# Kernel tuning notes

Hardware: AMD Instinct MI355X
Metric: run time of the kernel (lower is better)

The kernel has to match this reference:

```python
import jax, jax.numpy as jnp
import numpy as np
import math

HIDDEN = 1024
HEADS = 16
HEAD_DIM = HIDDEN // HEADS


def setup_inputs() -> dict:
    key = jax.random.key(0)
    ks = jax.random.split(key, 9)
    B, T, C = 4, 2048, HIDDEN
    s = 0.02
    x = jax.random.normal(ks[0], (B, T, C), dtype=jnp.float32)
    # torch nn.Linear weights are [out_features, in_features]
    Wq = jax.random.normal(ks[1], (C, C), dtype=jnp.float32) * s
    Wk = jax.random.normal(ks[2], (C, C), dtype=jnp.float32) * s
    Wv = jax.random.normal(ks[3], (C, C), dtype=jnp.float32) * s
    Wo = jax.random.normal(ks[4], (C, C), dtype=jnp.float32) * s
    bq = jax.random.normal(ks[5], (C,), dtype=jnp.float32) * s
    bk = jax.random.normal(ks[6], (C,), dtype=jnp.float32) * s
    bv = jax.random.normal(ks[7], (C,), dtype=jnp.float32) * s
    bo = jax.random.normal(ks[8], (C,), dtype=jnp.float32) * s
    return {"x": x, "Wq": Wq, "bq": bq, "Wk": Wk, "bk": bk,
            "Wv": Wv, "bv": bv, "Wo": Wo, "bo": bo}


def reference(x, Wq, bq, Wk, bk, Wv, bv, Wo, bo):
    B, T, C = x.shape
    H, D = HEADS, HEAD_DIM
    # projections: torch Linear => x @ W.T + b
    q = (x @ Wq.T + bq).reshape(B, T, H, D).transpose(0, 2, 1, 3)  # [B,H,T,D]
    k = (x @ Wk.T + bk).reshape(B, T, H, D).transpose(0, 2, 1, 3)
    v = (x @ Wv.T + bv).reshape(B, T, H, D).transpose(0, 2, 1, 3)
    scale = 1.0 / math.sqrt(D)
    scores = jnp.einsum('bhqd,bhkd->bhqk', q, k) * scale  # [B,H,T,T]
    attn = jax.nn.softmax(scores, axis=-1)
    y = jnp.einsum('bhqk,bhkd->bhqd', attn, v)  # [B,H,T,D]
    y = y.transpose(0, 2, 1, 3).reshape(B, T, C)
    return y @ Wo.T + bo
```

## Files before the change

### kernel.cpp

```cpp
#include <hip/hip_runtime.h>
#include <stdint.h>


using u16 = unsigned short;
using u32 = unsigned int;
typedef __attribute__((ext_vector_type(8)))  __bf16 bf16x8;
typedef __attribute__((ext_vector_type(4)))  float  floatx4;
typedef __attribute__((ext_vector_type(16))) float  f32x16;
typedef __attribute__((ext_vector_type(2)))  unsigned int u32x2;

#define QSCALE 0.18033688011112043f

__device__ __forceinline__ u16 f2b(float f) {
    union { float f; u32 i; } x; x.f = f;
    return (u16)((x.i + 0x7fffu + ((x.i >> 16) & 1u)) >> 16);
}
__device__ __forceinline__ u32 fbits(float f) { union { float f; u32 i; } x; x.f = f; return x.i; }
__device__ __forceinline__ u32 pkbf(float a, float b) {
    u32 ia = fbits(a) + 0x8000u, ib = fbits(b) + 0x8000u;
    return __builtin_amdgcn_perm(ib, ia, 0x07060302u);
}
__device__ __forceinline__ u32 cvtpk(float a, float b) {
    u32 r; asm("v_cvt_pk_bf16_f32 %0, %1, %2" : "=v"(r) : "v"(a), "v"(b)); return r;
}
__device__ __forceinline__ bf16x8 ld16B(const u16* p) {
    bf16x8 v; __builtin_memcpy(&v, p, 16); return v;
}
__device__ __forceinline__ void async16(const u16* g, u16* l) {
    __builtin_amdgcn_global_load_lds((const __attribute__((address_space(1))) unsigned int*)g,
                                     (__attribute__((address_space(3))) unsigned int*)l,
                                     16, 0, 0);
}

__global__ __launch_bounds__(256) void convert_kernel(
    const float* __restrict__ x,
    const float* __restrict__ Wq, const float* __restrict__ Wk,
    const float* __restrict__ Wv, const float* __restrict__ Wo,
    u16* __restrict__ xb, u16* __restrict__ wqb, u16* __restrict__ wkb,
    u16* __restrict__ wvb, u16* __restrict__ wob)
{
    size_t e = ((size_t)blockIdx.x * 256 + threadIdx.x) * 4;
    const float* src; u16* dst; size_t off;
    const size_t XN = (size_t)8 << 20;
    if (e < XN) { src = x; dst = xb; off = e; }
    else {
        size_t k = e - XN;
        int w = (int)(k >> 20);
        off = k & ((1u << 20) - 1);
        src = (w == 0) ? Wq : (w == 1) ? Wk : (w == 2) ? Wv : Wo;
        dst = (w == 0) ? wqb : (w == 1) ? wkb : (w == 2) ? wvb : wob;
    }
    float4 f = *(const float4*)(src + off);
    u32 dws[2] = { pkbf(f.x, f.y), pkbf(f.z, f.w) };
    __builtin_memcpy(dst + off, dws, 8);
}

__device__ __forceinline__ void gemm_loop(const u16* __restrict__ A, const u16* __restrict__ W,
                                          int m0, int n0, floatx4 (&acc)[4][4],
                                          u16* __restrict__ sA, u16* __restrict__ sB)
{
    constexpr int K = 1024;
    const int tid  = threadIdx.x;
    const int wave = tid >> 6, lane = tid & 63;
    const int wr = wave >> 1, wc = wave & 1;
    const int quad = lane >> 4, l15 = lane & 15;

    #pragma unroll
    for (int i = 0; i < 4; ++i)
        #pragma unroll
        for (int j = 0; j < 4; ++j)
            acc[i][j] = (floatx4){0.f, 0.f, 0.f, 0.f};

    const int rstage = lane >> 3;
    const int gstage = lane & 7;

    #pragma unroll 1
    for (int kb = 0; kb < 16; ++kb) {
        __syncthreads();
        const int k0 = kb * 64;
        #pragma unroll
        for (int j = 0; j < 4; ++j) {
            int r  = wave * 32 + j * 8 + rstage;
            int kg = gstage ^ (r & 7);
            async16(A + (size_t)(m0 + r) * K + k0 + kg * 8, &sA[(wave * 32 + j * 8) * 64]);
            async16(W + (size_t)(n0 + r) * K + k0 + kg * 8, &sB[(wave * 32 + j * 8) * 64]);
        }
        __syncthreads();

        #pragma unroll
        for (int kk = 0; kk < 2; ++kk) {
            bf16x8 af[4], bf[4];
            const int kg = kk * 4 + quad;
            #pragma unroll
            for (int t = 0; t < 4; ++t) {
                int ra = wr * 64 + t * 16 + l15;
                af[t] = ld16B(&sA[ra * 64 + ((kg ^ (ra & 7)) * 8)]);
                int rb = wc * 64 + t * 16 + l15;
                bf[t] = ld16B(&sB[rb * 64 + ((kg ^ (rb & 7)) * 8)]);
            }
            #pragma unroll
            for (int mt = 0; mt < 4; ++mt)
                #pragma unroll
                for (int nt = 0; nt < 4; ++nt)
                    acc[mt][nt] = __builtin_amdgcn_mfma_f32_16x16x32_bf16(af[mt], bf[nt], acc[mt][nt], 0, 0, 0);
        }
    }
}

__global__ __launch_bounds__(256, 3) void qkv_kernel(
    const u16* __restrict__ x, const u16* __restrict__ Wcat,
    const float* __restrict__ bq, const float* __restrict__ bk, const float* __restrict__ bv,
    u16* __restrict__ q, u16* __restrict__ k, u16* __restrict__ vt)
{
    __shared__ __align__(16) u16 sA[128 * 64];
    __shared__ __align__(16) u16 sB[128 * 64];
    const int id = blockIdx.x;
    const int xcd = id & 7, slot = id >> 3;
    const int m0 = (xcd * 8 + (slot & 7)) * 128;
    const int n0 = (slot >> 3) * 128;
    floatx4 acc[4][4];
    gemm_loop(x, Wcat, m0, n0, acc, sA, sB);

    const int tid = threadIdx.x;
    const int wave = tid >> 6, lane = tid & 63;
    const int wr = wave >> 1, wc = wave & 1;
    const int quad = lane >> 4, l15 = lane & 15;

    const int z = n0 >> 10;
    const float* bb = (z == 0) ? bq : (z == 1) ? bk : bv;
    const float scale = (z == 0) ? QSCALE : 1.0f;
    u16* o = (z == 0) ? q : k;

    #pragma unroll
    for (int nt = 0; nt < 4; ++nt) {
        int col  = n0 + wc * 64 + nt * 16 + l15;
        int c    = col & 1023;
        float bv_ = bb[c];
        #pragma unroll
        for (int mt = 0; mt < 4; ++mt) {
            int row0 = m0 + wr * 64 + mt * 16 + quad * 4;
            if (z == 2) {
                float v0 = acc[mt][nt][0] + bv_, v1 = acc[mt][nt][1] + bv_;
                float v2 = acc[mt][nt][2] + bv_, v3 = acc[mt][nt][3] + bv_;
                u32 dws[2] = { pkbf(v0, v1), pkbf(v2, v3) };
                int b = row0 >> 11, t0 = row0 & 2047;
                size_t idx = ((size_t)((b * 16 + (c >> 6)) * 64 + (c & 63)) * 2048) + t0;
                __builtin_memcpy(vt + idx, dws, 8);
            } else {
                #pragma unroll
                for (int r = 0; r < 4; ++r) {
                    float v = (acc[mt][nt][r] + bv_) * scale;
                    o[(size_t)(row0 + r) * 1024 + c] = f2b(v);
                }
            }
        }
    }
}

__global__ __launch_bounds__(256, 3) void proj_kernel(
    const u16* __restrict__ y, const u16* __restrict__ Wo, const float* __restrict__ bo,
    float* __restrict__ out)
{
    __shared__ __align__(16) u16 sA[128 * 64];
    __shared__ __align__(16) u16 sB[128 * 64];
    const int id = blockIdx.x;
    const int xcd = id & 7, slot = id >> 3;
    const int m0 = (xcd * 8 + (slot & 7)) * 128;
    const int n0 = (slot >> 3) * 128;
    floatx4 acc[4][4];
    gemm_loop(y, Wo, m0, n0, acc, sA, sB);

    const int tid = threadIdx.x;
    const int wave = tid >> 6, lane = tid & 63;
    const int wr = wave >> 1, wc = wave & 1;
    const int quad = lane >> 4, l15 = lane & 15;

    #pragma unroll
    for (int nt = 0; nt < 4; ++nt) {
        int col = n0 + wc * 64 + nt * 16 + l15;
        float bv_ = bo[col];
        #pragma unroll
        for (int mt = 0; mt < 4; ++mt) {
            int row0 = m0 + wr * 64 + mt * 16 + quad * 4;
            #pragma unroll
            for (int r = 0; r < 4; ++r)
                out[(size_t)(row0 + r) * 1024 + col] = acc[mt][nt][r] + bv_;
        }
    }
}

__global__ __launch_bounds__(256, 2) void attn_kernel(
    const u16* __restrict__ Q, const u16* __restrict__ K,
    const u16* __restrict__ Vt, u16* __restrict__ Y)
{
    const int bh = blockIdx.x, qt = blockIdx.y;
    const int tid = threadIdx.x;
    const int wave = tid >> 6, lane = tid & 63;
    const int hf = lane >> 5, l31 = lane & 31, l7 = l31 & 7;
    const int b = bh >> 4, h = bh & 15;

    __shared__ __align__(16) u16 smem[16384];

    bf16x8 qf[2][4];
    {
        const size_t q0 = (size_t)(b * 2048 + qt * 256 + wave * 64) * 1024 + h * 64 + hf * 8;
        #pragma unroll
        for (int nq = 0; nq < 2; ++nq)
            #pragma unroll
            for (int dc = 0; dc < 4; ++dc)
                qf[nq][dc] = ld16B(Q + q0 + (size_t)(nq * 32 + l31) * 1024 + dc * 16);
    }

    const int r8 = lane >> 3;
    const int g7 = (lane & 7) ^ r8;
    const u16* ksrc = K + (size_t)(b * 2048 + wave * 16 + r8) * 1024 + h * 64 + g7 * 8;
    const u16* vbase = Vt + (size_t)(bh * 64 + l31) * 2048 + hf * 8;

    f32x16 accO[2][2];
    #pragma unroll
    for (int dt = 0; dt < 2; ++dt)
        #pragma unroll
        for (int nq = 0; nq < 2; ++nq)
            #pragma unroll
            for (int i = 0; i < 16; ++i) accO[dt][nq][i] = 0.f;
    float accS[2] = {0.f, 0.f};
    const f32x16 fz = {0.f,0.f,0.f,0.f,0.f,0.f,0.f,0.f,0.f,0.f,0.f,0.f,0.f,0.f,0.f,0.f};

    {
        u16* dK = smem + wave * 1024;
        async16(ksrc,            dK);
        async16(ksrc + 8 * 1024, dK + 512);
    }
    __syncthreads();

    #pragma unroll 1
    for (int kt = 0; kt < 32; ++kt) {
        const int cur = kt & 1;

        bf16x8 vfm[2][4];
        {
            const u16* vbl = vbase + kt * 64;
            #pragma unroll
            for (int dt = 0; dt < 2; ++dt)
                #pragma unroll
                for (int c = 0; c < 4; ++c)
                    vfm[dt][c] = ld16B(vbl + (size_t)dt * 32 * 2048 + c * 16);
        }

        if (kt < 31) {
            u16* dK = smem + (cur ^ 1) * 4096 + wave * 1024;
            const u16* ks = ksrc + (size_t)(kt + 1) * 64 * 1024;
            async16(ks,            dK);
            async16(ks + 8 * 1024, dK + 512);
        }

        const u16* bK = smem + cur * 4096;
        bf16x8 kfm[2][4];
        #pragma unroll
        for (int m = 0; m < 2; ++m) {
            const int row = m * 32 + l31;
            #pragma unroll
            for (int dc = 0; dc < 4; ++dc)
                kfm[m][dc] = ld16B(&bK[row * 64 + (((dc * 2 + hf) ^ l7) * 8)]);
        }

        f32x16 st[2][2];
        __builtin_amdgcn_s_setprio(1);
        #pragma unroll
        for (int m = 0; m < 2; ++m)
            #pragma unroll
            for (int nq = 0; nq < 2; ++nq)
                st[m][nq] = __builtin_amdgcn_mfma_f32_32x32x16_bf16(kfm[m][0], qf[nq][0], fz, 0, 0, 0);
        #pragma unroll
        for (int dc = 1; dc < 4; ++dc)
            #pragma unroll
            for (int m = 0; m < 2; ++m)
                #pragma unroll
                for (int nq = 0; nq < 2; ++nq)
                    st[m][nq] = __builtin_amdgcn_mfma_f32_32x32x16_bf16(kfm[m][dc], qf[nq][dc], st[m][nq], 0, 0, 0);
        __builtin_amdgcn_s_setprio(0);

        #pragma unroll
        for (int c = 0; c < 4; ++c) {
            const int m = c >> 1, r0 = (c & 1) * 8;
            #pragma unroll
            for (int nq = 0; nq < 2; ++nq) {
                float e0 = __builtin_amdgcn_exp2f(st[m][nq][r0 + 0]);
                float e1 = __builtin_amdgcn_exp2f(st[m][nq][r0 + 1]);
                float e2 = __builtin_amdgcn_exp2f(st[m][nq][r0 + 2]);
                float e3 = __builtin_amdgcn_exp2f(st[m][nq][r0 + 3]);
                float e4 = __builtin_amdgcn_exp2f(st[m][nq][r0 + 4]);
                float e5 = __builtin_amdgcn_exp2f(st[m][nq][r0 + 5]);
                float e6 = __builtin_amdgcn_exp2f(st[m][nq][r0 + 6]);
                float e7 = __builtin_amdgcn_exp2f(st[m][nq][r0 + 7]);
                accS[nq] += ((e0 + e1) + (e2 + e3)) + ((e4 + e5) + (e6 + e7));
                u32 Ua = cvtpk(e0, e1), Ub = cvtpk(e2, e3);
                u32 Va = cvtpk(e4, e5), Vb = cvtpk(e6, e7);
                u32x2 s0 = __builtin_amdgcn_permlane32_swap(Ua, Va, false, false);
                u32x2 s1 = __builtin_amdgcn_permlane32_swap(Ub, Vb, false, false);
                u32 dws[4] = { s0.x, s1.x, s0.y, s1.y };
                bf16x8 pB; __builtin_memcpy(&pB, dws, 16);
                __builtin_amdgcn_s_setprio(1);
                accO[0][nq] = __builtin_amdgcn_mfma_f32_32x32x16_bf16(vfm[0][c], pB, accO[0][nq], 0, 0, 0);
                accO[1][nq] = __builtin_amdgcn_mfma_f32_32x32x16_bf16(vfm[1][c], pB, accO[1][nq], 0, 0, 0);
                __builtin_amdgcn_s_setprio(0);
            }
        }
        __syncthreads();
    }

    #pragma unroll
    for (int nq = 0; nq < 2; ++nq) accS[nq] += __shfl_xor(accS[nq], 32);
    const float inv0 = 1.f / accS[0], inv1 = 1.f / accS[1];

    u16* ep = smem + wave * 4096;
    #pragma unroll
    for (int nq = 0; nq < 2; ++nq) {
        const float inv = nq ? inv1 : inv0;
        const int row = nq * 32 + l31;
        #pragma unroll
        for (int dt = 0; dt < 2; ++dt)
            #pragma unroll
            for (int rq = 0; rq < 4; ++rq) {
                float v0 = accO[dt][nq][rq * 4 + 0] * inv;
                float v1 = accO[dt][nq][rq * 4 + 1] * inv;
                float v2 = accO[dt][nq][rq * 4 + 2] * inv;
                float v3 = accO[dt][nq][rq * 4 + 3] * inv;
                u32 dws[2] = { cvtpk(v0, v1), cvtpk(v2, v3) };
                const int g = dt * 4 + rq;
                __builtin_memcpy((char*)ep + row * 128 + ((g ^ l7) * 16) + hf * 8, dws, 8);
            }
    }
    const int rl = lane >> 3, cl = lane & 7;
    #pragma unroll
    for (int pass = 0; pass < 8; ++pass) {
        const int row = pass * 8 + rl;
        bf16x8 vrow = ld16B((const u16*)((const char*)ep + row * 128 + ((cl ^ (row & 7)) * 16)));
        const int t = qt * 256 + wave * 64 + row;
        __builtin_memcpy(Y + ((size_t)(b * 2048 + t)) * 1024 + h * 64 + cl * 8, &vrow, 16);
    }
}

extern "C" void kernel_launch(void* const* d_in, const int* in_sizes, int n_in,
                              void* d_out, int out_size, void* d_ws, size_t ws_size,
                              hipStream_t stream)
{
    const float* x  = (const float*)d_in[0];
    const float* Wq = (const float*)d_in[1];
    const float* bq = (const float*)d_in[2];
    const float* Wk = (const float*)d_in[3];
    const float* bk = (const float*)d_in[4];
    const float* Wv = (const float*)d_in[5];
    const float* bv = (const float*)d_in[6];
    const float* Wo = (const float*)d_in[7];
    const float* bo = (const float*)d_in[8];
    float* out = (float*)d_out;

    const size_t NTOK = (size_t)8192 * 1024;
    const size_t WN   = (size_t)1024 * 1024;
    u16* xb  = (u16*)d_ws;
    u16* wqb = xb + NTOK;
    u16* wkb = wqb + WN;
    u16* wvb = wkb + WN;
    u16* wob = wvb + WN;
    u16* q   = wob + WN;
    u16* k   = q + NTOK;
    u16* vt  = k + NTOK;
    u16* y   = vt + NTOK;

    convert_kernel<<<dim3(12288), 256, 0, stream>>>(x, Wq, Wk, Wv, Wo, xb, wqb, wkb, wvb, wob);
    qkv_kernel<<<dim3(1536), 256, 0, stream>>>(xb, wqb, bq, bk, bv, q, k, vt);
    attn_kernel<<<dim3(64, 8), 256, 0, stream>>>(q, k, vt, y);
    proj_kernel<<<dim3(512), 256, 0, stream>>>(y, wob, bo, out);
}
```

Before: 274.6 us.

## Software-pipeline attention: stage V through LDS and overlap next QK^T with softmax·V

```diff
diff --git a/kernel.cpp b/kernel.cpp
--- a/kernel.cpp
+++ b/kernel.cpp
@@ -189,6 +189,79 @@
     }
 }
 
+
+#define S_TILE(stD, bK)                                                             \
+    do {                                                                            \
+        bf16x8 kfm[2][4];                                                           \
+        _Pragma("unroll")                                                           \
+        for (int m_ = 0; m_ < 2; ++m_) {                                            \
+            const int row_ = m_ * 32 + l31;                                         \
+            _Pragma("unroll")                                                       \
+            for (int dc_ = 0; dc_ < 4; ++dc_)                                       \
+                kfm[m_][dc_] = ld16B(&(bK)[row_ * 64 + (((dc_ * 2 + hf) ^ l7) * 8)]); \
+        }                                                                           \
+        __builtin_amdgcn_s_setprio(1);                                              \
+        _Pragma("unroll")                                                           \
+        for (int m_ = 0; m_ < 2; ++m_)                                              \
+            _Pragma("unroll")                                                       \
+            for (int nq_ = 0; nq_ < 2; ++nq_)                                       \
+                stD[m_][nq_] = __builtin_amdgcn_mfma_f32_32x32x16_bf16(kfm[m_][0], qf[nq_][0], fz, 0, 0, 0); \
+        _Pragma("unroll")                                                           \
+        for (int dc_ = 1; dc_ < 4; ++dc_)                                           \
+            _Pragma("unroll")                                                       \
+            for (int m_ = 0; m_ < 2; ++m_)                                          \
+                _Pragma("unroll")                                                   \
+                for (int nq_ = 0; nq_ < 2; ++nq_)                                   \
+                    stD[m_][nq_] = __builtin_amdgcn_mfma_f32_32x32x16_bf16(kfm[m_][dc_], qf[nq_][dc_], stD[m_][nq_], 0, 0, 0); \
+        __builtin_amdgcn_s_setprio(0);                                              \
+    } while (0)
+
+#define EXP_PV(stP, bV)                                                             \
+    do {                                                                            \
+        bf16x8 vfm[2][4];                                                           \
+        _Pragma("unroll")                                                           \
+        for (int dt_ = 0; dt_ < 2; ++dt_) {                                         \
+            const int row_ = dt_ * 32 + l31;                                        \
+            _Pragma("unroll")                                                       \
+            for (int c_ = 0; c_ < 4; ++c_)                                          \
+                vfm[dt_][c_] = ld16B(&(bV)[row_ * 64 + (((c_ * 2 + hf) ^ l7) * 8)]); \
+        }                                                                           \
+        _Pragma("unroll")                                                           \
+        for (int c_ = 0; c_ < 4; ++c_) {                                            \
+            const int m_ = c_ >> 1, r0_ = (c_ & 1) * 8;                             \
+            _Pragma("unroll")                                                       \
+            for (int nq_ = 0; nq_ < 2; ++nq_) {                                     \
+                float e0 = __builtin_amdgcn_exp2f(stP[m_][nq_][r0_ + 0]);           \
+                float e1 = __builtin_amdgcn_exp2f(stP[m_][nq_][r0_ + 1]);           \
+                float e2 = __builtin_amdgcn_exp2f(stP[m_][nq_][r0_ + 2]);           \
+                float e3 = __builtin_amdgcn_exp2f(stP[m_][nq_][r0_ + 3]);           \
+                float e4 = __builtin_amdgcn_exp2f(stP[m_][nq_][r0_ + 4]);           \
+                float e5 = __builtin_amdgcn_exp2f(stP[m_][nq_][r0_ + 5]);           \
+                float e6 = __builtin_amdgcn_exp2f(stP[m_][nq_][r0_ + 6]);           \
+                float e7 = __builtin_amdgcn_exp2f(stP[m_][nq_][r0_ + 7]);           \
+                accS[nq_] += ((e0 + e1) + (e2 + e3)) + ((e4 + e5) + (e6 + e7));     \
+                u32 Ua = cvtpk(e0, e1), Ub = cvtpk(e2, e3);                         \
+                u32 Va = cvtpk(e4, e5), Vb = cvtpk(e6, e7);                         \
+                u32x2 s0 = __builtin_amdgcn_permlane32_swap(Ua, Va, false, false);  \
+                u32x2 s1 = __builtin_amdgcn_permlane32_swap(Ub, Vb, false, false);  \
+                u32 dws_[4] = { s0.x, s1.x, s0.y, s1.y };                           \
+                bf16x8 pB; __builtin_memcpy(&pB, dws_, 16);                         \
+                __builtin_amdgcn_s_setprio(1);                                      \
+                accO[0][nq_] = __builtin_amdgcn_mfma_f32_32x32x16_bf16(vfm[0][c_], pB, accO[0][nq_], 0, 0, 0); \
+                accO[1][nq_] = __builtin_amdgcn_mfma_f32_32x32x16_bf16(vfm[1][c_], pB, accO[1][nq_], 0, 0, 0); \
+                __builtin_amdgcn_s_setprio(0);                                      \
+            }                                                                       \
+        }                                                                           \
+    } while (0)
+
+#define ATTN_STEP(stP, stN, t)                                                      \
+    do {                                                                            \
+        __syncthreads();         \
+        if ((t) < 30) { stageK((t) + 2); stageV((t) + 2); }                         \
+        EXP_PV(stP, sV + ((t) % 3) * 4096);                                         \
+        S_TILE(stN, sK + (((t) + 1) & 1) * 4096);                                   \
+    } while (0)
+
 __global__ __launch_bounds__(256, 2) void attn_kernel(
     const u16* __restrict__ Q, const u16* __restrict__ K,
     const u16* __restrict__ Vt, u16* __restrict__ Y)
@@ -199,7 +272,9 @@
     const int hf = lane >> 5, l31 = lane & 31, l7 = l31 & 7;
     const int b = bh >> 4, h = bh & 15;
 
-    __shared__ __align__(16) u16 smem[16384];
+    __shared__ __align__(16) u16 smem[20480];
+    u16* sK = smem;
+    u16* sV = smem + 8192;
 
     bf16x8 qf[2][4];
     {
@@ -213,8 +288,21 @@
 
     const int r8 = lane >> 3;
     const int g7 = (lane & 7) ^ r8;
-    const u16* ksrc = K + (size_t)(b * 2048 + wave * 16 + r8) * 1024 + h * 64 + g7 * 8;
-    const u16* vbase = Vt + (size_t)(bh * 64 + l31) * 2048 + hf * 8;
+    const u16* ksrc = K  + (size_t)(b * 2048 + wave * 16 + r8) * 1024 + h * 64 + g7 * 8;
+    const u16* vsrc = Vt + ((size_t)(bh * 64 + wave * 16 + r8)) * 2048 + g7 * 8;
+
+    auto stageK = [&](int t) {
+        u16* dK = sK + (t & 1) * 4096 + wave * 1024;
+        const u16* ks = ksrc + (size_t)t * 64 * 1024;
+        async16(ks,            dK);
+        async16(ks + 8 * 1024, dK + 512);
+    };
+    auto stageV = [&](int t) {
+        u16* dV = sV + (t % 3) * 4096 + wave * 1024;
+        const u16* vs = vsrc + (size_t)t * 64;
+        async16(vs,            dV);
+        async16(vs + 8 * 2048, dV + 512);
+    };
 
     f32x16 accO[2][2];
     #pragma unroll
@@ -226,92 +314,27 @@
     float accS[2] = {0.f, 0.f};
     const f32x16 fz = {0.f,0.f,0.f,0.f,0.f,0.f,0.f,0.f,0.f,0.f,0.f,0.f,0.f,0.f,0.f,0.f};
 
-    {
-        u16* dK = smem + wave * 1024;
-        async16(ksrc,            dK);
-        async16(ksrc + 8 * 1024, dK + 512);
-    }
+    stageK(0); stageV(0);
     __syncthreads();
+    stageK(1); stageV(1);
+
+    f32x16 stA[2][2], stB[2][2];
+    S_TILE(stA, sK);
 
     #pragma unroll 1
-    for (int kt = 0; kt < 32; ++kt) {
-        const int cur = kt & 1;
-
-        bf16x8 vfm[2][4];
-        {
-            const u16* vbl = vbase + kt * 64;
-            #pragma unroll
-            for (int dt = 0; dt < 2; ++dt)
-                #pragma unroll
-                for (int c = 0; c < 4; ++c)
-                    vfm[dt][c] = ld16B(vbl + (size_t)dt * 32 * 2048 + c * 16);
-        }
-
-        if (kt < 31) {
-            u16* dK = smem + (cur ^ 1) * 4096 + wave * 1024;
-            const u16* ks = ksrc + (size_t)(kt + 1) * 64 * 1024;
-            async16(ks,            dK);
-            async16(ks + 8 * 1024, dK + 512);
-        }
-
-        const u16* bK = smem + cur * 4096;
-        bf16x8 kfm[2][4];
-        #pragma unroll
-        for (int m = 0; m < 2; ++m) {
-            const int row = m * 32 + l31;
-            #pragma unroll
-            for (int dc = 0; dc < 4; ++dc)
-                kfm[m][dc] = ld16B(&bK[row * 64 + (((dc * 2 + hf) ^ l7) * 8)]);
-        }
-
-        f32x16 st[2][2];
-        __builtin_amdgcn_s_setprio(1);
-        #pragma unroll
-        for (int m = 0; m < 2; ++m)
-            #pragma unroll
-            for (int nq = 0; nq < 2; ++nq)
-                st[m][nq] = __builtin_amdgcn_mfma_f32_32x32x16_bf16(kfm[m][0], qf[nq][0], fz, 0, 0, 0);
-        #pragma unroll
-        for (int dc = 1; dc < 4; ++dc)
-            #pragma unroll
-            for (int m = 0; m < 2; ++m)
-                #pragma unroll
-                for (int nq = 0; nq < 2; ++nq)
-                    st[m][nq] = __builtin_amdgcn_mfma_f32_32x32x16_bf16(kfm[m][dc], qf[nq][dc], st[m][nq], 0, 0, 0);
-        __builtin_amdgcn_s_setprio(0);
-
-        #pragma unroll
-        for (int c = 0; c < 4; ++c) {
-            const int m = c >> 1, r0 = (c & 1) * 8;
-            #pragma unroll
-            for (int nq = 0; nq < 2; ++nq) {
-                float e0 = __builtin_amdgcn_exp2f(st[m][nq][r0 + 0]);
-                float e1 = __builtin_amdgcn_exp2f(st[m][nq][r0 + 1]);
-                float e2 = __builtin_amdgcn_exp2f(st[m][nq][r0 + 2]);
-                float e3 = __builtin_amdgcn_exp2f(st[m][nq][r0 + 3]);
-                float e4 = __builtin_amdgcn_exp2f(st[m][nq][r0 + 4]);
-                float e5 = __builtin_amdgcn_exp2f(st[m][nq][r0 + 5]);
-                float e6 = __builtin_amdgcn_exp2f(st[m][nq][r0 + 6]);
-                float e7 = __builtin_amdgcn_exp2f(st[m][nq][r0 + 7]);
-                accS[nq] += ((e0 + e1) + (e2 + e3)) + ((e4 + e5) + (e6 + e7));
-                u32 Ua = cvtpk(e0, e1), Ub = cvtpk(e2, e3);
-                u32 Va = cvtpk(e4, e5), Vb = cvtpk(e6, e7);
-                u32x2 s0 = __builtin_amdgcn_permlane32_swap(Ua, Va, false, false);
-                u32x2 s1 = __builtin_amdgcn_permlane32_swap(Ub, Vb, false, false);
-                u32 dws[4] = { s0.x, s1.x, s0.y, s1.y };
-                bf16x8 pB; __builtin_memcpy(&pB, dws, 16);
-                __builtin_amdgcn_s_setprio(1);
-                accO[0][nq] = __builtin_amdgcn_mfma_f32_32x32x16_bf16(vfm[0][c], pB, accO[0][nq], 0, 0, 0);
-                accO[1][nq] = __builtin_amdgcn_mfma_f32_32x32x16_bf16(vfm[1][c], pB, accO[1][nq], 0, 0, 0);
-                __builtin_amdgcn_s_setprio(0);
-            }
-        }
-        __syncthreads();
-    }
+    for (int t2 = 0; t2 < 30; t2 += 2) {
+        ATTN_STEP(stA, stB, t2);
+        ATTN_STEP(stB, stA, t2 + 1);
+    }
+    ATTN_STEP(stA, stB, 30);
+
+    EXP_PV(stB, sV + (31 % 3) * 4096);
 
     #pragma unroll
     for (int nq = 0; nq < 2; ++nq) accS[nq] += __shfl_xor(accS[nq], 32);
     const float inv0 = 1.f / accS[0], inv1 = 1.f / accS[1];
+
+    __syncthreads();
 
     u16* ep = smem + wave * 4096;
     #pragma unroll
```

Result: faster. 244.8 us (-10.8%).
